# Performance work log

Measured on AMD Instinct MI355X. Metric: run time of the kernel, lower is better.

Reference implementation:

```python
import jax, jax.numpy as jnp
import numpy as np

BSIZE = 1024
DIM = 16384
HID = 1024
R = 8  # module init arg: radius in torch.randint(1, 2R)


def setup_inputs() -> dict:
    key = jax.random.key(0)
    k1, k2, k3, k4, k5 = jax.random.split(key, 5)
    # binary state in {0,1}
    x = (jax.random.uniform(k1, (BSIZE, DIM)) < 0.5).astype(jnp.float32)
    # RBM-style energy model params (the external `model` in the torch code)
    W = jax.random.normal(k2, (DIM, HID), dtype=jnp.float32) * 0.01
    bh = jax.random.normal(k3, (HID,), dtype=jnp.float32) * 0.01
    c = jax.random.normal(k4, (DIM,), dtype=jnp.float32) * 0.01
    # radius ~ Uniform{1, ..., 2R-1}, as torch.randint(1, 2R)
    radius = jax.random.randint(k5, (BSIZE,), 1, 2 * R)
    return {"x": x, "W": W, "bh": bh, "c": c, "radius": radius}


def reference(x, W, bh, c, radius):
    max_r = 2 * R - 1  # static upper bound; r_mask zeroes out steps >= radius[b]
    bsize, dim = x.shape

    def model(z):  # per-sample score, shape [bsize]
        return jnp.sum(jax.nn.softplus(z @ W + bh), axis=-1) + z @ c

    score_x = model(x)
    # grad_x is detached in the torch code
    grad_x = jax.lax.stop_gradient(jax.grad(lambda z: model(z).sum())(x))

    r_mask = (jnp.arange(max_r)[None, :] < radius[:, None]).astype(x.dtype)  # [bsize, max_r]
    # log_Zx computed at step 0 where cur_x == x
    log_Zx = jax.nn.logsumexp(-(2.0 * x - 1.0) * grad_x * 0.5, axis=-1)

    b_idx = jnp.arange(bsize)
    base_key = jax.random.key(42)

    def body(cur_x, step):
        # softmax over score_change + multinomial draw == categorical over logits
        logits = -(2.0 * cur_x - 1.0) * grad_x * 0.5
        idx = jax.random.categorical(jax.random.fold_in(base_key, step), logits)  # [bsize]
        cur_bits = cur_x[b_idx, idx]
        m = r_mask[:, step]
        new_vals = m * (1.0 - cur_bits) + (1.0 - m) * cur_bits
        cur_x = cur_x.at[b_idx, idx].set(new_vals)
        return cur_x, None

    y, _ = jax.lax.scan(body, x, jnp.arange(max_r))

    score_y = model(y)
    log_pypx = score_y - score_x
    log_tilde_pxpy = -jnp.sum(grad_x * (y - x), axis=-1)
    log_zxzy = log_Zx - jax.nn.logsumexp(-(2.0 * y - 1.0) * grad_x * 0.5, axis=-1)
    log_acc = jnp.minimum(log_pypx + log_tilde_pxpy + log_zxzy, 0.0)

    u = jax.random.uniform(jax.random.fold_in(base_key, max_r + 1), (bsize,))
    accepted = (jnp.exp(log_acc) >= u).astype(x.dtype)[:, None]  # [bsize, 1]
    return y * accepted + (1.0 - accepted) * x
```

## Files before the change

kernel.cpp:

```cpp
#include <hip/hip_runtime.h>
#include <stdint.h>

#define BSIZE 1024
#define DIM   16384
#define HID   1024
#define SPLITK 8
#define KC     (DIM / SPLITK)
#define NT    1024
#define SV    (DIM / NT)
#define NBKT  1024

__device__ __forceinline__ void tf2x32(uint32_t k0, uint32_t k1,
                                       uint32_t x0, uint32_t x1,
                                       uint32_t& o0, uint32_t& o1) {
  const uint32_t ks2 = k0 ^ k1 ^ 0x1BD11BDAu;
#define TFR(r) { x0 += x1; x1 = (x1 << r) | (x1 >> (32 - r)); x1 ^= x0; }
  x0 += k0; x1 += k1;
  TFR(13) TFR(15) TFR(26) TFR(6)
  x0 += k1;  x1 += ks2 + 1u;
  TFR(17) TFR(29) TFR(16) TFR(24)
  x0 += ks2; x1 += k0 + 2u;
  TFR(13) TFR(15) TFR(26) TFR(6)
  x0 += k0;  x1 += k1 + 3u;
  TFR(17) TFR(29) TFR(16) TFR(24)
  x0 += k1;  x1 += ks2 + 4u;
  TFR(13) TFR(15) TFR(26) TFR(6)
  x0 += ks2; x1 += k0 + 5u;
#undef TFR
  o0 = x0; o1 = x1;
}

__device__ __forceinline__ float bits_to_unit_float(uint32_t bits) {
  return __uint_as_float((bits >> 9) | 0x3f800000u) - 1.0f;
}

__device__ __forceinline__ float bits_to_gumbel(uint32_t bits) {
  float u = bits_to_unit_float(bits);
  if (u == 0.0f) u = 1.1754943508222875e-38f;
  float l1 = (float)log((double)u);
  float nl1 = -l1;
  float l2 = (float)log((double)nl1);
  return -l2;
}

__device__ __forceinline__ double softplus_d(double z) {
  return (z > 0.0) ? (z + log1p(exp(-z))) : log1p(exp(z));
}

__global__ __launch_bounds__(256) void fill_gbounds_kernel(
    float* __restrict__ gminb, float* __restrict__ gmaxb) {
  const uint32_t i = blockIdx.x * 256 + threadIdx.x;
  const uint32_t mlo = i << 13;
  const uint32_t mhi = mlo + 8191u;
  gminb[i] = bits_to_gumbel(mlo << 9);
  gmaxb[i] = bits_to_gumbel(mhi << 9);
}

__global__ __launch_bounds__(256) void gemm_h_split_kernel(
    const float* __restrict__ x, const float* __restrict__ W,
    float* __restrict__ P) {
  __shared__ float Al[32][128];
  __shared__ float Bl[32][128];
  const int tid = threadIdx.x;
  const int n0 = blockIdx.x * 128;
  const int m0 = blockIdx.y * 128;
  const int s  = blockIdx.z;
  const int arow = tid >> 1, akof = (tid & 1) * 16;
  const int brow = tid >> 3, bcol = (tid & 7) * 16;
  const int ty = tid >> 4, tx = tid & 15;

  float acc[8][8];
  for (int i = 0; i < 8; ++i)
    for (int j = 0; j < 8; ++j) acc[i][j] = 0.0f;

  for (int kt = 0; kt < KC / 32; ++kt) {
    const int k0 = s * KC + kt * 32;
    const float* ap = x + (size_t)(m0 + arow) * DIM + k0 + akof;
    float4 av0 = *(const float4*)(ap + 0);
    float4 av1 = *(const float4*)(ap + 4);
    float4 av2 = *(const float4*)(ap + 8);
    float4 av3 = *(const float4*)(ap + 12);
    const float* bp = W + (size_t)(k0 + brow) * HID + n0 + bcol;
    float4 bv0 = *(const float4*)(bp + 0);
    float4 bv1 = *(const float4*)(bp + 4);
    float4 bv2 = *(const float4*)(bp + 8);
    float4 bv3 = *(const float4*)(bp + 12);
    __syncthreads();
    {
      float ta[16] = {av0.x,av0.y,av0.z,av0.w, av1.x,av1.y,av1.z,av1.w,
                      av2.x,av2.y,av2.z,av2.w, av3.x,av3.y,av3.z,av3.w};
      for (int e = 0; e < 16; ++e) Al[akof + e][arow] = ta[e];
    }
    *(float4*)&Bl[brow][bcol + 0]  = bv0;
    *(float4*)&Bl[brow][bcol + 4]  = bv1;
    *(float4*)&Bl[brow][bcol + 8]  = bv2;
    *(float4*)&Bl[brow][bcol + 12] = bv3;
    __syncthreads();
#pragma unroll 4
    for (int k = 0; k < 32; ++k) {
      const float4 a0 = *(const float4*)&Al[k][ty * 8];
      const float4 a1 = *(const float4*)&Al[k][ty * 8 + 4];
      const float4 b0 = *(const float4*)&Bl[k][tx * 8];
      const float4 b1 = *(const float4*)&Bl[k][tx * 8 + 4];
      const float a[8]  = {a0.x,a0.y,a0.z,a0.w, a1.x,a1.y,a1.z,a1.w};
      const float bb[8] = {b0.x,b0.y,b0.z,b0.w, b1.x,b1.y,b1.z,b1.w};
      for (int i = 0; i < 8; ++i)
        for (int j = 0; j < 8; ++j)
          acc[i][j] = fmaf(a[i], bb[j], acc[i][j]);
    }
  }
  float* Cp = P + (size_t)s * (BSIZE * HID);
  for (int i = 0; i < 8; ++i) {
    const int gm = m0 + ty * 8 + i;
    float4 w0 = {acc[i][0], acc[i][1], acc[i][2], acc[i][3]};
    float4 w1 = {acc[i][4], acc[i][5], acc[i][6], acc[i][7]};
    *(float4*)(Cp + (size_t)gm * HID + n0 + tx * 8 + 0) = w0;
    *(float4*)(Cp + (size_t)gm * HID + n0 + tx * 8 + 4) = w1;
  }
}

__global__ __launch_bounds__(256) void reduce_h_sig_kernel(
    const float* __restrict__ P, const float* __restrict__ bh,
    float* __restrict__ hbuf, float* __restrict__ sig) {
  const int i = blockIdx.x * 256 + threadIdx.x;
  float4 a = ((const float4*)P)[i];
  for (int s = 1; s < SPLITK; ++s) {
    float4 p = ((const float4*)P)[(size_t)s * (BSIZE * HID / 4) + i];
    a.x += p.x; a.y += p.y; a.z += p.z; a.w += p.w;
  }
  float4 bv = ((const float4*)bh)[i & (HID / 4 - 1)];
  float4 h;
  h.x = a.x + bv.x; h.y = a.y + bv.y; h.z = a.z + bv.z; h.w = a.w + bv.w;
  ((float4*)hbuf)[i] = h;
  float4 sg;
  sg.x = (float)(1.0 / (1.0 + exp(-(double)h.x)));
  sg.y = (float)(1.0 / (1.0 + exp(-(double)h.y)));
  sg.z = (float)(1.0 / (1.0 + exp(-(double)h.z)));
  sg.w = (float)(1.0 / (1.0 + exp(-(double)h.w)));
  ((float4*)sig)[i] = sg;
}

__global__ __launch_bounds__(256) void gemm2_sig128_kernel(
    const float* __restrict__ sig_src, const float* __restrict__ W,
    const float* __restrict__ c, const float* __restrict__ x,
    float* __restrict__ s_dst) {
  __shared__ float Al[32][128];
  __shared__ float Bl[32][128];
  const int tid = threadIdx.x;
  const int m0 = blockIdx.x * 128;
  const int n0 = blockIdx.y * 128;
  const int row2 = tid >> 1, kof = (tid & 1) * 16;
  const int ty = tid >> 4, tx = tid & 15;

  float acc[8][8];
  for (int i = 0; i < 8; ++i)
    for (int j = 0; j < 8; ++j) acc[i][j] = 0.0f;

  for (int kt = 0; kt < HID / 32; ++kt) {
    const int k0 = kt * 32;
    const float* ap = sig_src + (size_t)(m0 + row2) * HID + k0 + kof;
    float4 av0 = *(const float4*)(ap + 0);
    float4 av1 = *(const float4*)(ap + 4);
    float4 av2 = *(const float4*)(ap + 8);
    float4 av3 = *(const float4*)(ap + 12);
    const float* bp = W + (size_t)(n0 + row2) * HID + k0 + kof;
    float4 bv0 = *(const float4*)(bp + 0);
    float4 bv1 = *(const float4*)(bp + 4);
    float4 bv2 = *(const float4*)(bp + 8);
    float4 bv3 = *(const float4*)(bp + 12);
    __syncthreads();
    {
      float ta[16] = {av0.x,av0.y,av0.z,av0.w, av1.x,av1.y,av1.z,av1.w,
                      av2.x,av2.y,av2.z,av2.w, av3.x,av3.y,av3.z,av3.w};
      float tb[16] = {bv0.x,bv0.y,bv0.z,bv0.w, bv1.x,bv1.y,bv1.z,bv1.w,
                      bv2.x,bv2.y,bv2.z,bv2.w, bv3.x,bv3.y,bv3.z,bv3.w};
      for (int e = 0; e < 16; ++e) { Al[kof + e][row2] = ta[e]; Bl[kof + e][row2] = tb[e]; }
    }
    __syncthreads();
#pragma unroll 4
    for (int k = 0; k < 32; ++k) {
      const float4 a0 = *(const float4*)&Al[k][ty * 8];
      const float4 a1 = *(const float4*)&Al[k][ty * 8 + 4];
      const float4 b0 = *(const float4*)&Bl[k][tx * 8];
      const float4 b1 = *(const float4*)&Bl[k][tx * 8 + 4];
      const float a[8]  = {a0.x,a0.y,a0.z,a0.w, a1.x,a1.y,a1.z,a1.w};
      const float bb[8] = {b0.x,b0.y,b0.z,b0.w, b1.x,b1.y,b1.z,b1.w};
      for (int i = 0; i < 8; ++i)
        for (int j = 0; j < 8; ++j)
          acc[i][j] = fmaf(a[i], bb[j], acc[i][j]);
    }
  }
  for (int i = 0; i < 8; ++i) {
    const int gm = m0 + ty * 8 + i;
    const size_t rowoff = (size_t)gm * DIM + n0 + tx * 8;
    for (int q = 0; q < 2; ++q) {
      float4 xv = *(const float4*)(x + rowoff + q * 4);
      float4 cv = *(const float4*)(c + n0 + tx * 8 + q * 4);
      float g0 = acc[i][q * 4 + 0] + cv.x;
      float g1 = acc[i][q * 4 + 1] + cv.y;
      float g2 = acc[i][q * 4 + 2] + cv.z;
      float g3 = acc[i][q * 4 + 3] + cv.w;
      float4 sv;
      sv.x = ((xv.x == 1.0f) ? -g0 : g0) * 0.5f;
      sv.y = ((xv.y == 1.0f) ? -g1 : g1) * 0.5f;
      sv.z = ((xv.z == 1.0f) ? -g2 : g2) * 0.5f;
      sv.w = ((xv.w == 1.0f) ? -g3 : g3) * 0.5f;
      *(float4*)(s_dst + rowoff + q * 4) = sv;
    }
  }
}

__global__ __launch_bounds__(512) void row_kernel_f(
    const float* __restrict__ x, const float* __restrict__ W,
    const float* __restrict__ c, const int* __restrict__ radius,
    const float* __restrict__ h_base,
    const float* __restrict__ s_base,
    const float* __restrict__ gminb, const float* __restrict__ gmaxb,
    float* __restrict__ out) {
  const int b = blockIdx.x;
  const int tid = threadIdx.x;

  __shared__ float  gmin_l[NBKT];
  __shared__ float  gmax_l[NBKT];
  __shared__ float  red_v[8];
  __shared__ int    red_i[8];
  __shared__ double red_d[8];
  __shared__ int    diff[16];
  __shared__ float  sgn_sh[16];
  __shared__ float  sflip[16];
  __shared__ int    diff_cnt;
  __shared__ int    accept_flag;

  if (tid == 0) diff_cnt = 0;
  gmin_l[tid]       = gminb[tid];
  gmin_l[tid + 512] = gminb[tid + 512];
  gmax_l[tid]       = gmaxb[tid];
  gmax_l[tid + 512] = gmaxb[tid + 512];

  float sv[32];
#pragma unroll
  for (int i = 0; i < 32; ++i)
    sv[i] = s_base[(size_t)b * DIM + tid + i * 512];
  __syncthreads();

  auto block_lse = [&]() -> double {
    float mloc = sv[0];
#pragma unroll
    for (int i = 1; i < 32; ++i) mloc = fmaxf(mloc, sv[i]);
    for (int o = 32; o; o >>= 1) mloc = fmaxf(mloc, __shfl_xor(mloc, o));
    if ((tid & 63) == 0) red_v[tid >> 6] = mloc;
    __syncthreads();
    const float m = fmaxf(fmaxf(fmaxf(red_v[0], red_v[1]), fmaxf(red_v[2], red_v[3])),
                          fmaxf(fmaxf(red_v[4], red_v[5]), fmaxf(red_v[6], red_v[7])));
    double ssum = 0.0;
#pragma unroll
    for (int i = 0; i < 32; ++i) ssum += exp((double)sv[i] - (double)m);
    for (int o = 32; o; o >>= 1) ssum += __shfl_xor(ssum, o);
    if ((tid & 63) == 0) red_d[tid >> 6] = ssum;
    __syncthreads();
    double tot = ((red_d[0] + red_d[1]) + (red_d[2] + red_d[3])) +
                 ((red_d[4] + red_d[5]) + (red_d[6] + red_d[7]));
    __syncthreads();
    return log(tot) + (double)m;
  };

  const double logZx = block_lse();

  int r = radius[b];
  if (r < 0) r = 0;
  if (r > 15) r = 15;
  const uint32_t jbase = (uint32_t)(b * DIM);

  for (int t = 0; t < r; ++t) {
    uint32_t kt0, kt1;
    tf2x32(0u, 42u, 0u, (uint32_t)t, kt0, kt1);

    float lbmax = -3.402823466e38f;
#pragma unroll
    for (int i = 0; i < 32; ++i) {
      const int d = tid + (i << 9);
      uint32_t o0, o1;
      tf2x32(kt0, kt1, 0u, jbase + (uint32_t)d, o0, o1);
      const uint32_t bits = o0 ^ o1;
      lbmax = fmaxf(lbmax, gmin_l[bits >> 22] + sv[i]);
    }
    for (int o = 32; o; o >>= 1) lbmax = fmaxf(lbmax, __shfl_xor(lbmax, o));
    if ((tid & 63) == 0) red_v[tid >> 6] = lbmax;
    __syncthreads();
    const float L = fmaxf(fmaxf(fmaxf(red_v[0], red_v[1]), fmaxf(red_v[2], red_v[3])),
                          fmaxf(fmaxf(red_v[4], red_v[5]), fmaxf(red_v[6], red_v[7])));
    __syncthreads();

    float bestv = -3.402823466e38f;
    int   besti = 0x7fffffff;
#pragma unroll
    for (int i = 0; i < 32; ++i) {
      const int d = tid + (i << 9);
      uint32_t o0, o1;
      tf2x32(kt0, kt1, 0u, jbase + (uint32_t)d, o0, o1);
      const uint32_t bits = o0 ^ o1;
      if (gmax_l[bits >> 22] + sv[i] >= L) {
        const float val = bits_to_gumbel(bits) + sv[i];
        if (val > bestv) { bestv = val; besti = d; }
      }
    }
    for (int o = 32; o; o >>= 1) {
      const float ov = __shfl_xor(bestv, o);
      const int   oi = __shfl_xor(besti, o);
      if (ov > bestv || (ov == bestv && oi < besti)) { bestv = ov; besti = oi; }
    }
    if ((tid & 63) == 0) { red_v[tid >> 6] = bestv; red_i[tid >> 6] = besti; }
    __syncthreads();
    float bv = red_v[0]; int bi = red_i[0];
    for (int w = 1; w < 8; ++w)
      if (red_v[w] > bv || (red_v[w] == bv && red_i[w] < bi)) { bv = red_v[w]; bi = red_i[w]; }
    if ((bi & 511) == tid) {
      const int slot = bi >> 9;
#pragma unroll
      for (int i = 0; i < 32; ++i) if (i == slot) sv[i] = -sv[i];
    }
    if (tid == 0) {
      int found = -1;
      for (int j = 0; j < diff_cnt; ++j) if (diff[j] == bi) found = j;
      if (found >= 0) { diff[found] = diff[diff_cnt - 1]; diff_cnt -= 1; }
      else { diff[diff_cnt] = bi; diff_cnt += 1; }
    }
    __syncthreads();
  }

  const double lse_y = block_lse();

  const int dc_n = diff_cnt;
  for (int j = 0; j < dc_n; ++j) {
    const int d = diff[j];
    if ((d & 511) == tid) {
      const int slot = d >> 9;
#pragma unroll
      for (int i = 0; i < 32; ++i) if (i == slot) sflip[j] = sv[i];
    }
  }
  if (tid < dc_n) sgn_sh[tid] = 1.0f - 2.0f * x[(size_t)b * DIM + diff[tid]];
  __syncthreads();

  double dsp = 0.0;
  for (int rep = 0; rep < 2; ++rep) {
    const int hh = tid + rep * 512;
    const float hxv = h_base[(size_t)b * HID + hh];
    double delta = 0.0;
    for (int j = 0; j < dc_n; ++j)
      delta += (double)sgn_sh[j] * (double)W[(size_t)diff[j] * HID + hh];
    if (dc_n > 0) {
      const double hx = (double)hxv;
      dsp += softplus_d(hx + delta) - softplus_d(hx);
    }
  }
  for (int o = 32; o; o >>= 1) dsp += __shfl_xor(dsp, o);
  if ((tid & 63) == 0) red_d[tid >> 6] = dsp;
  __syncthreads();

  if (tid == 0) {
    const double dsp_tot = ((red_d[0] + red_d[1]) + (red_d[2] + red_d[3])) +
                           ((red_d[4] + red_d[5]) + (red_d[6] + red_d[7]));
    double dc = 0.0, ltilde = 0.0;
    for (int j = 0; j < dc_n; ++j) {
      dc += (double)sgn_sh[j] * (double)c[diff[j]];
      ltilde += 2.0 * (double)sflip[j];
    }
    double la = (dsp_tot + dc) + ltilde + (logZx - lse_y);
    if (la > 0.0) la = 0.0;
    const double p = exp(la);
    uint32_t ku0, ku1, o0, o1;
    tf2x32(0u, 42u, 0u, 16u, ku0, ku1);
    tf2x32(ku0, ku1, 0u, (uint32_t)b, o0, o1);
    const float ub = bits_to_unit_float(o0 ^ o1);
    accept_flag = (p >= (double)ub) ? 1 : 0;
  }
  __syncthreads();

  {
    const float4* xr = (const float4*)(x + (size_t)b * DIM);
    float4* orow = (float4*)(out + (size_t)b * DIM);
    for (int i = 0; i < DIM / 4 / 512; ++i)
      orow[i * 512 + tid] = xr[i * 512 + tid];
  }
  __syncthreads();
  if (accept_flag && tid < dc_n) {
    const int d = diff[tid];
    out[(size_t)b * DIM + d] = 1.0f - x[(size_t)b * DIM + d];
  }
}

__global__ __launch_bounds__(1024) void row_kernel_w(
    const float* __restrict__ x, const float* __restrict__ W,
    const float* __restrict__ c, const int* __restrict__ radius,
    const float* __restrict__ h_base, const float* __restrict__ s_base,
    float* __restrict__ out) {
  const int b = blockIdx.x;
  const int tid = threadIdx.x;

  __shared__ float  red_v[16];
  __shared__ int    red_i[16];
  __shared__ double red_d[16];
  __shared__ int    diff[16];
  __shared__ float  sgn_sh[16];
  __shared__ float  sflip[16];
  __shared__ int    diff_cnt;
  __shared__ int    accept_flag;

  if (tid == 0) diff_cnt = 0;

  float sv[SV];
#pragma unroll
  for (int i = 0; i < SV; ++i)
    sv[i] = s_base[(size_t)b * DIM + tid + i * NT];

  auto tree16f = [&](const float* v) -> float {
    return fmaxf(fmaxf(fmaxf(fmaxf(v[0],v[1]),fmaxf(v[2],v[3])),
                       fmaxf(fmaxf(v[4],v[5]),fmaxf(v[6],v[7]))),
                 fmaxf(fmaxf(fmaxf(v[8],v[9]),fmaxf(v[10],v[11])),
                       fmaxf(fmaxf(v[12],v[13]),fmaxf(v[14],v[15]))));
  };
  auto tree16d = [&](const double* v) -> double {
    return ((((v[0]+v[1])+(v[2]+v[3])) + ((v[4]+v[5])+(v[6]+v[7])))
          + (((v[8]+v[9])+(v[10]+v[11])) + ((v[12]+v[13])+(v[14]+v[15]))));
  };

  auto block_lse = [&]() -> double {
    float mloc = sv[0];
#pragma unroll
    for (int i = 1; i < SV; ++i) mloc = fmaxf(mloc, sv[i]);
    for (int o = 32; o; o >>= 1) mloc = fmaxf(mloc, __shfl_xor(mloc, o));
    if ((tid & 63) == 0) red_v[tid >> 6] = mloc;
    __syncthreads();
    const float m = tree16f(red_v);
    double ssum = 0.0;
#pragma unroll
    for (int i = 0; i < SV; ++i) ssum += exp((double)sv[i] - (double)m);
    for (int o = 32; o; o >>= 1) ssum += __shfl_xor(ssum, o);
    if ((tid & 63) == 0) red_d[tid >> 6] = ssum;
    __syncthreads();
    double tot = tree16d(red_d);
    __syncthreads();
    return log(tot) + (double)m;
  };

  const double logZx = block_lse();

  int r = radius[b];
  if (r < 0) r = 0;
  if (r > 15) r = 15;
  const uint32_t jbase = (uint32_t)(b * DIM);

  for (int t = 0; t < r; ++t) {
    uint32_t kt0, kt1;
    tf2x32(0u, 42u, 0u, (uint32_t)t, kt0, kt1);
    float bestv;
    int   besti;
    {
      uint32_t o0, o1;
      tf2x32(kt0, kt1, 0u, jbase + (uint32_t)tid, o0, o1);
      bestv = bits_to_gumbel(o0 ^ o1) + sv[0];
      besti = tid;
    }
#pragma unroll
    for (int i = 1; i < SV; ++i) {
      const int d = tid + i * NT;
      uint32_t o0, o1;
      tf2x32(kt0, kt1, 0u, jbase + (uint32_t)d, o0, o1);
      const float val = bits_to_gumbel(o0 ^ o1) + sv[i];
      if (val > bestv) { bestv = val; besti = d; }
    }
    for (int o = 32; o; o >>= 1) {
      const float ov = __shfl_xor(bestv, o);
      const int   oi = __shfl_xor(besti, o);
      if (ov > bestv || (ov == bestv && oi < besti)) { bestv = ov; besti = oi; }
    }
    if ((tid & 63) == 0) { red_v[tid >> 6] = bestv; red_i[tid >> 6] = besti; }
    __syncthreads();
    float bv = red_v[0]; int bi = red_i[0];
    for (int w = 1; w < 16; ++w)
      if (red_v[w] > bv || (red_v[w] == bv && red_i[w] < bi)) { bv = red_v[w]; bi = red_i[w]; }
    if ((bi & (NT - 1)) == tid) {
      const int slot = bi >> 10;
#pragma unroll
      for (int i = 0; i < SV; ++i) if (i == slot) sv[i] = -sv[i];
    }
    if (tid == 0) {
      int found = -1;
      for (int j = 0; j < diff_cnt; ++j) if (diff[j] == bi) found = j;
      if (found >= 0) { diff[found] = diff[diff_cnt - 1]; diff_cnt -= 1; }
      else { diff[diff_cnt] = bi; diff_cnt += 1; }
    }
    __syncthreads();
  }

  const double lse_y = block_lse();

  const int dc_n = diff_cnt;
  for (int j = 0; j < dc_n; ++j) {
    const int d = diff[j];
    if ((d & (NT - 1)) == tid) {
      const int slot = d >> 10;
#pragma unroll
      for (int i = 0; i < SV; ++i) if (i == slot) sflip[j] = sv[i];
    }
  }
  if (tid < dc_n) sgn_sh[tid] = 1.0f - 2.0f * x[(size_t)b * DIM + diff[tid]];
  __syncthreads();

  double dsp = 0.0;
  {
    const int hh = tid;
    const float hxv = h_base[(size_t)b * HID + hh];
    double delta = 0.0;
    for (int j = 0; j < dc_n; ++j)
      delta += (double)sgn_sh[j] * (double)W[(size_t)diff[j] * HID + hh];
    if (dc_n > 0) {
      const double hx = (double)hxv;
      dsp += softplus_d(hx + delta) - softplus_d(hx);
    }
  }
  for (int o = 32; o; o >>= 1) dsp += __shfl_xor(dsp, o);
  if ((tid & 63) == 0) red_d[tid >> 6] = dsp;
  __syncthreads();

  if (tid == 0) {
    const double dsp_tot = tree16d(red_d);
    double dc = 0.0, ltilde = 0.0;
    for (int j = 0; j < dc_n; ++j) {
      dc += (double)sgn_sh[j] * (double)c[diff[j]];
      ltilde += 2.0 * (double)sflip[j];
    }
    double la = (dsp_tot + dc) + ltilde + (logZx - lse_y);
    if (la > 0.0) la = 0.0;
    const double p = exp(la);
    uint32_t ku0, ku1, o0, o1;
    tf2x32(0u, 42u, 0u, 16u, ku0, ku1);
    tf2x32(ku0, ku1, 0u, (uint32_t)b, o0, o1);
    const float ub = bits_to_unit_float(o0 ^ o1);
    accept_flag = (p >= (double)ub) ? 1 : 0;
  }
  __syncthreads();

  {
    const float4* xr = (const float4*)(x + (size_t)b * DIM);
    float4* orow = (float4*)(out + (size_t)b * DIM);
    for (int i = 0; i < DIM / 4 / NT; ++i)
      orow[i * NT + tid] = xr[i * NT + tid];
  }
  __syncthreads();
  if (accept_flag && tid < dc_n) {
    const int d = diff[tid];
    out[(size_t)b * DIM + d] = 1.0f - x[(size_t)b * DIM + d];
  }
}

extern "C" void kernel_launch(void* const* d_in, const int* in_sizes, int n_in,
                              void* d_out, int out_size, void* d_ws, size_t ws_size,
                              hipStream_t stream) {
  const float* x      = (const float*)d_in[0];
  const float* W      = (const float*)d_in[1];
  const float* bh     = (const float*)d_in[2];
  const float* c      = (const float*)d_in[3];
  const int*   radius = (const int*)d_in[4];
  float* out = (float*)d_out;
  const size_t F = sizeof(float);

  if (ws_size < (size_t)2 * BSIZE * HID * F) return;

  float* h_ws   = (float*)d_ws;
  float* sig_ws = h_ws + (size_t)BSIZE * HID;
  float* P      = out;

  dim3 g1(HID / 128, BSIZE / 128, SPLITK);
  gemm_h_split_kernel<<<g1, 256, 0, stream>>>(x, W, P);

  reduce_h_sig_kernel<<<(BSIZE * HID / 4) / 256, 256, 0, stream>>>(P, bh, h_ws, sig_ws);

  dim3 g2(BSIZE / 128, DIM / 128);
  gemm2_sig128_kernel<<<g2, 256, 0, stream>>>(sig_ws, W, c, x, out);

  if (ws_size >= ((size_t)2 * BSIZE * HID + 2 * NBKT) * F) {
    float* gminb = sig_ws + (size_t)BSIZE * HID;
    float* gmaxb = gminb + NBKT;
    fill_gbounds_kernel<<<NBKT / 256, 256, 0, stream>>>(gminb, gmaxb);
    row_kernel_f<<<BSIZE, 512, 0, stream>>>(x, W, c, radius, h_ws, out,
                                            gminb, gmaxb, out);
  } else {
    row_kernel_w<<<BSIZE, NT, 0, stream>>>(x, W, c, radius, h_ws, out, out);
  }
}
```

Baseline: 1.733 ms.

## Schedule row blocks longest-radius-first and cache Threefry bits between passes

```diff
diff --git a/kernel.cpp b/kernel.cpp
--- a/kernel.cpp
+++ b/kernel.cpp
@@ -56,6 +56,23 @@
   gmaxb[i] = bits_to_gumbel(mhi << 9);
 }
 
+__global__ __launch_bounds__(1024) void sort_perm_kernel(
+    const int* __restrict__ radius, int* __restrict__ perm) {
+  __shared__ int rad[BSIZE];
+  const int i = threadIdx.x;
+  int r = radius[i];
+  if (r < 0) r = 0;
+  if (r > 15) r = 15;
+  rad[i] = r;
+  __syncthreads();
+  int rank = 0;
+  for (int j = 0; j < BSIZE; ++j) {
+    const int rj = rad[j];
+    rank += (rj > r) || (rj == r && j < i);
+  }
+  perm[rank] = i;
+}
+
 __global__ __launch_bounds__(256) void gemm_h_split_kernel(
     const float* __restrict__ x, const float* __restrict__ W,
     float* __restrict__ P) {
@@ -216,8 +233,9 @@
     const float* __restrict__ h_base,
     const float* __restrict__ s_base,
     const float* __restrict__ gminb, const float* __restrict__ gmaxb,
+    const int* __restrict__ perm,
     float* __restrict__ out) {
-  const int b = blockIdx.x;
+  const int b = perm[blockIdx.x];
   const int tid = threadIdx.x;
 
   __shared__ float  gmin_l[NBKT];
@@ -275,14 +293,15 @@
     uint32_t kt0, kt1;
     tf2x32(0u, 42u, 0u, (uint32_t)t, kt0, kt1);
 
+    uint32_t bb[32];
     float lbmax = -3.402823466e38f;
 #pragma unroll
     for (int i = 0; i < 32; ++i) {
       const int d = tid + (i << 9);
       uint32_t o0, o1;
       tf2x32(kt0, kt1, 0u, jbase + (uint32_t)d, o0, o1);
-      const uint32_t bits = o0 ^ o1;
-      lbmax = fmaxf(lbmax, gmin_l[bits >> 22] + sv[i]);
+      bb[i] = o0 ^ o1;
+      lbmax = fmaxf(lbmax, gmin_l[bb[i] >> 22] + sv[i]);
     }
     for (int o = 32; o; o >>= 1) lbmax = fmaxf(lbmax, __shfl_xor(lbmax, o));
     if ((tid & 63) == 0) red_v[tid >> 6] = lbmax;
@@ -296,9 +315,7 @@
 #pragma unroll
     for (int i = 0; i < 32; ++i) {
       const int d = tid + (i << 9);
-      uint32_t o0, o1;
-      tf2x32(kt0, kt1, 0u, jbase + (uint32_t)d, o0, o1);
-      const uint32_t bits = o0 ^ o1;
+      const uint32_t bits = bb[i];
       if (gmax_l[bits >> 22] + sv[i] >= L) {
         const float val = bits_to_gumbel(bits) + sv[i];
         if (val > bestv) { bestv = val; besti = d; }
@@ -580,12 +597,14 @@
   dim3 g2(BSIZE / 128, DIM / 128);
   gemm2_sig128_kernel<<<g2, 256, 0, stream>>>(sig_ws, W, c, x, out);
 
-  if (ws_size >= ((size_t)2 * BSIZE * HID + 2 * NBKT) * F) {
+  if (ws_size >= ((size_t)2 * BSIZE * HID + 2 * NBKT + BSIZE) * F) {
     float* gminb = sig_ws + (size_t)BSIZE * HID;
     float* gmaxb = gminb + NBKT;
+    int*   perm  = (int*)(gmaxb + NBKT);
     fill_gbounds_kernel<<<NBKT / 256, 256, 0, stream>>>(gminb, gmaxb);
+    sort_perm_kernel<<<1, BSIZE, 0, stream>>>(radius, perm);
     row_kernel_f<<<BSIZE, 512, 0, stream>>>(x, W, c, radius, h_ws, out,
-                                            gminb, gmaxb, out);
+                                            gminb, gmaxb, perm, out);
   } else {
     row_kernel_w<<<BSIZE, NT, 0, stream>>>(x, W, c, radius, h_ws, out, out);
   }
```

Result: faster. 1.407 ms (median of 2 runs) (-18.9%).
